# Kernel optimization log

Hardware: AMD Instinct MI355X
Metric: run time of the kernel (lower is better)

Reference implementation:

```python
import jax, jax.numpy as jnp
import numpy as np

ORDER = 256
THETA = 1024.0
HIDDEN = 512
FEAT = 128
BATCH = 64
SEQ = 1025  # loop consumes steps 1..SEQ-1 -> T = 1024 outputs
LEAKY_SLOPE = 0.2  # tf.nn.leaky_relu default alpha


def _expm_np(M):
    # scaling-and-squaring + Taylor, float64, sufficient for the LMU A matrix
    n = max(0, int(np.ceil(np.log2(max(1.0, np.linalg.norm(M, 1))))) + 4)
    A = M / (2.0 ** n)
    E = np.eye(M.shape[0])
    term = np.eye(M.shape[0])
    for k in range(1, 24):
        term = term @ A / k
        E = E + term
    for _ in range(n):
        E = E @ E
    return E


def get_state_space_matrices(order, theta):
    Q = np.arange(order, dtype=np.float64)
    R = (2 * Q + 1)[:, None] / theta
    j, i = np.meshgrid(Q, Q)
    Ac = np.where(i < j, -1, (-1.0) ** (i - j + 1)) * R
    Bc = (-1.0) ** Q[:, None] * R
    # zero-order-hold discretization with dt=1 (matches scipy cont2discrete zoh)
    Ad = _expm_np(Ac)
    Bd = np.linalg.solve(Ac, (Ad - np.eye(order)) @ Bc)
    return Ad.astype(np.float32), Bd.astype(np.float32)


def _glorot(key, shape):
    fan_in, fan_out = shape[0], shape[1]
    lim = np.sqrt(6.0 / (fan_in + fan_out))
    return jax.random.uniform(key, shape, jnp.float32, -lim, lim)


def setup_inputs() -> dict:
    key = jax.random.key(0)
    ks = jax.random.split(key, 6)
    A_np, B_np = get_state_space_matrices(ORDER, THETA)
    return {
        "x": jax.random.normal(ks[0], (BATCH, SEQ, FEAT), jnp.float32),
        "A": jnp.asarray(A_np),            # (order, order)
        "Bv": jnp.asarray(B_np),           # (order, 1)
        "W_x": _glorot(ks[1], (FEAT, HIDDEN)),
        "e_x": _glorot(ks[2], (FEAT, 1)),
        "W_h": _glorot(ks[3], (HIDDEN, HIDDEN)),
        "W_m": _glorot(ks[4], (HIDDEN, ORDER)),
    }


def reference(x, A, Bv, W_x, e_x, W_h, W_m):
    B, S, F = x.shape
    order = A.shape[0]
    hidden_dim = W_h.shape[0]
    b_row = Bv[:, 0]  # (order,)

    def step(carry, x_t):
        m, h = carry                       # m: (B, order), h: (B, hidden)
        u = x_t @ e_x                      # (B, 1)
        m = m @ A.T + b_row[None, :] * u   # A@m + B*u  -> (B, order)
        h = x_t @ W_x + h @ W_h.T + m @ W_m.T
        h = jnp.where(h >= 0, h, LEAKY_SLOPE * h)  # leaky_relu(alpha=0.2)
        return (m, h), h

    m0 = jnp.zeros((B, order), jnp.float32)
    h0 = jnp.zeros((B, hidden_dim), jnp.float32)
    xs = jnp.swapaxes(x[:, 1:, :], 0, 1)   # (T, B, F); step 0 is skipped as in the source
    _, hs = jax.lax.scan(step, (m0, h0), xs)
    return jnp.swapaxes(hs, 0, 1)          # (B, T, hidden)
```

## Files before the change

### kernel.cpp

```cpp
#include <hip/hip_runtime.h>
#include <stdint.h>


typedef _Float16 half8 __attribute__((ext_vector_type(8)));
typedef float f32x4 __attribute__((ext_vector_type(4)));
typedef unsigned int u32x4 __attribute__((ext_vector_type(4)));
typedef unsigned int u32x2 __attribute__((ext_vector_type(2)));

union H8 { half8 h; unsigned int u[4]; };
union F16 { u32x4 q; half8 h; };

#define MFMA16(a, b, c) __builtin_amdgcn_mfma_f32_16x16x32_f16((a), (b), (c), 0, 0, 0)
#define ASTORE64(p, v) __hip_atomic_store((unsigned long long*)(p), (v), \
                                          __ATOMIC_RELAXED, __HIP_MEMORY_SCOPE_AGENT)

__device__ __forceinline__ half8 ld_frag16(const _Float16* W, size_t foff) {
    F16 r;
    r.q = *(const u32x4*)(W + foff);
    return r.h;
}

__device__ __forceinline__ void unpack8(u32x4 A, u32x4 B, half8& hi, half8& lo) {
    H8 h, l;
    h.u[0] = (A[0] & 0xffffu) | (A[1] << 16);  l.u[0] = (A[0] >> 16) | (A[1] & 0xffff0000u);
    h.u[1] = (A[2] & 0xffffu) | (A[3] << 16);  l.u[1] = (A[2] >> 16) | (A[3] & 0xffff0000u);
    h.u[2] = (B[0] & 0xffffu) | (B[1] << 16);  l.u[2] = (B[0] >> 16) | (B[1] & 0xffff0000u);
    h.u[3] = (B[2] & 0xffffu) | (B[3] << 16);  l.u[3] = (B[2] >> 16) | (B[3] & 0xffff0000u);
    hi = h.h; lo = l.h;
}

__global__ void k_prep(const float* __restrict__ A, const float* __restrict__ W_x,
                       const float* __restrict__ W_h, const float* __restrict__ W_m,
                       _Float16* __restrict__ Whi, _Float16* __restrict__ Wlo,
                       _Float16* __restrict__ WxThi, _Float16* __restrict__ WxTlo,
                       float* __restrict__ WmT, float* __restrict__ AT) {
    int bid = blockIdx.x, tid = threadIdx.x;
    if (bid < 512) {
        int r = bid;
        for (int c = tid; c < 512; c += 256) {
            float v = W_h[(size_t)r * 512 + c];
            _Float16 hi = (_Float16)v;
            _Float16 lo = (_Float16)(v - (float)hi);
            int cb = c >> 5, w = c & 31;
            int kgi = (w & 15) >> 2;
            int e = (w & 3) + ((w & 16) ? 4 : 0);
            size_t idx = (((size_t)r * 16 + cb) * 4 + kgi) * 8 + e;
            Whi[idx] = hi;
            Wlo[idx] = lo;
        }
    } else if (bid < 1024) {
        int n = bid - 512;
        if (tid < 128) {
            int f = tid;
            float v = W_x[(size_t)f * 512 + n];
            _Float16 hi = (_Float16)v;
            _Float16 lo = (_Float16)(v - (float)hi);
            int kt = f >> 5, w = f & 31;
            int kgi = (w & 15) >> 2;
            int e = (w & 3) + ((w & 16) ? 4 : 0);
            size_t idx = (((size_t)n * 4 + kt) * 4 + kgi) * 8 + e;
            WxThi[idx] = hi;
            WxTlo[idx] = lo;
        }
    } else if (bid < 1280) {
        int d = bid - 1024;
        for (int n = tid; n < 512; n += 256)
            WmT[(size_t)d * 512 + n] = W_m[(size_t)n * 256 + d];
    } else {
        int e = bid - 1280;
        if (tid < 256) AT[(size_t)e * 256 + tid] = A[(size_t)tid * 256 + e];
    }
}

__global__ void k_u(const float* __restrict__ x, const float* __restrict__ e_x,
                    float* __restrict__ u) {
    int wave = threadIdx.x >> 6, l = threadIdx.x & 63;
    int t = blockIdx.x * 4 + wave;
    int b = blockIdx.y;
    const float* xr = x + ((size_t)b * 1025 + t + 1) * 128;
    float s = xr[2 * l] * e_x[2 * l] + xr[2 * l + 1] * e_x[2 * l + 1];
#pragma unroll
    for (int off = 1; off < 64; off <<= 1) s += __shfl_xor(s, off);
    if (l == 0) u[(size_t)b * 1024 + t] = s;
}

__global__ void k_a64(const float* __restrict__ S, float* __restrict__ D,
                      float* __restrict__ DT, int writeT) {
    int r = blockIdx.x, c = threadIdx.x;
    float acc = 0.f;
    for (int e = 0; e < 256; ++e)
        acc += S[(size_t)r * 256 + e] * S[(size_t)e * 256 + c];
    D[(size_t)r * 256 + c] = acc;
    if (writeT) DT[(size_t)c * 256 + r] = acc;
}

__global__ void k_vk(const float* __restrict__ AT, const float* __restrict__ Bv,
                     float* __restrict__ V) {
    __shared__ float cur[256];
    int tid = threadIdx.x;
    cur[tid] = Bv[tid];
    V[tid] = cur[tid];
    __syncthreads();
    for (int k = 1; k < 64; ++k) {
        float nv = 0.f;
        for (int e = 0; e < 256; ++e) nv += AT[(size_t)e * 256 + tid] * cur[e];
        __syncthreads();
        cur[tid] = nv;
        V[(size_t)k * 256 + tid] = nv;
        __syncthreads();
    }
}

__global__ void k_vchain(const float* __restrict__ A64T, float* __restrict__ V) {
    __shared__ float cur[256];
    int j = blockIdx.x, d = threadIdx.x;
    cur[d] = V[(size_t)j * 256 + d];
    __syncthreads();
    for (int c = 1; c < 16; ++c) {
        float nv = 0.f;
        for (int e = 0; e < 256; ++e) nv += A64T[(size_t)e * 256 + d] * cur[e];
        __syncthreads();
        cur[d] = nv;
        V[((size_t)c * 64 + j) * 256 + d] = nv;
        __syncthreads();
    }
}

__global__ void k_c(const float* __restrict__ V, const float* __restrict__ WmT,
                    _Float16* __restrict__ CThi) {
    int k = blockIdx.x, n = threadIdx.x;
    const float* vk = V + (size_t)k * 256;
    float acc = 0.f;
    for (int d = 0; d < 256; ++d) acc += vk[d] * WmT[(size_t)d * 512 + n];
    int ck = k >> 5, w = k & 31;
    int kgi = (w & 15) >> 2;
    int e = (w & 3) + ((w & 16) ? 4 : 0);
    CThi[(((size_t)n * 32 + ck) * 4 + kgi) * 8 + e] = (_Float16)acc;
}

__global__ __launch_bounds__(256, 1) void k_preconv(const float* __restrict__ x,
                                                    const float* __restrict__ u,
                                                    const _Float16* __restrict__ WxThi,
                                                    const _Float16* __restrict__ WxTlo,
                                                    const _Float16* __restrict__ CThi,
                                                    float* __restrict__ out) {
    __shared__ float xt[64][132];
    __shared__ float ut[1088];
    int tid = threadIdx.x;
    int Mb = blockIdx.x, Nb = blockIdx.y;
    int b = Mb >> 4;
    int t0 = (Mb & 15) * 64;
    const float* src = x + ((size_t)b * 1025 + t0 + 1) * 128;
#pragma unroll
    for (int i = 0; i < 8; ++i) {
        int idx = tid + i * 256;
        int row = idx >> 5, c4 = (idx & 31) * 4;
        *(f32x4*)&xt[row][c4] = *(const f32x4*)(src + (size_t)row * 128 + c4);
    }
    for (int i = tid; i < 1088; i += 256) {
        int tau = t0 - 1024 + i;
        ut[i] = (tau >= 0) ? u[(size_t)b * 1024 + tau] : 0.f;
    }
    __syncthreads();

    int wave = tid >> 6, l = tid & 63;
    int kg4 = l >> 4, kg = kg4 * 4;
    int mrow = wave * 16 + (l & 15);

    half8 ah[4], al[4];
#pragma unroll
    for (int kt = 0; kt < 4; ++kt) {
        f32x4 f0 = *(const f32x4*)&xt[mrow][kt * 32 + kg];
        f32x4 f1 = *(const f32x4*)&xt[mrow][kt * 32 + kg + 16];
        H8 hh, ll;
#pragma unroll
        for (int e = 0; e < 4; ++e) {
            _Float16 h0 = (_Float16)f0[e];
            ((_Float16*)&hh)[e] = h0;
            ((_Float16*)&ll)[e] = (_Float16)(f0[e] - (float)h0);
            _Float16 h1 = (_Float16)f1[e];
            ((_Float16*)&hh)[e + 4] = h1;
            ((_Float16*)&ll)[e + 4] = (_Float16)(f1[e] - (float)h1);
        }
        ah[kt] = hh.h;
        al[kt] = ll.h;
    }

    f32x4 acc[16];
#pragma unroll
    for (int nt = 0; nt < 16; ++nt) acc[nt] = (f32x4)0.f;

#pragma unroll
    for (int nt = 0; nt < 16; ++nt) {
        size_t nrow = (size_t)(Nb * 256 + nt * 16 + (l & 15));
#pragma unroll
        for (int kt = 0; kt < 4; ++kt) {
            size_t fo = (((nrow * 4 + kt) * 4 + kg4)) * 8;
            half8 bh = ld_frag16(WxThi, fo);
            half8 bl = ld_frag16(WxTlo, fo);
            acc[nt] = MFMA16(ah[kt], bh, acc[nt]);
            acc[nt] = MFMA16(al[kt], bh, acc[nt]);
            acc[nt] = MFMA16(ah[kt], bl, acc[nt]);
        }
    }

    for (int ck = 0; ck < 32; ++ck) {
        int base0 = mrow + 1024 - ck * 32 - kg;
        H8 au;
#pragma unroll
        for (int e = 0; e < 4; ++e) {
            ((_Float16*)&au)[e] = (_Float16)ut[base0 - e];
            ((_Float16*)&au)[e + 4] = (_Float16)ut[base0 - 16 - e];
        }
#pragma unroll
        for (int nt = 0; nt < 16; ++nt) {
            size_t nrow = (size_t)(Nb * 256 + nt * 16 + (l & 15));
            half8 bh = ld_frag16(CThi, (((nrow * 32 + ck) * 4 + kg4)) * 8);
            acc[nt] = MFMA16(au.h, bh, acc[nt]);
        }
    }

#pragma unroll
    for (int nt = 0; nt < 16; ++nt) {
#pragma unroll
        for (int r = 0; r < 4; ++r) {
            size_t bt = (size_t)Mb * 64 + wave * 16 + 4 * (l >> 4) + r;
            out[bt * 512 + Nb * 256 + nt * 16 + (l & 15)] = acc[nt][r];
        }
    }
}

#define TSTATE_U32 (64 * 512 * 2)

#define LD8W(p, v0, v1, v2, v3, v4, v5, v6, v7)                                   \
    asm volatile("global_load_dwordx4 %0, %8, off\n\t"                            \
                 "global_load_dwordx4 %1, %8, off offset:64\n\t"                  \
                 "global_load_dwordx4 %2, %8, off offset:128\n\t"                 \
                 "global_load_dwordx4 %3, %8, off offset:192\n\t"                 \
                 "global_load_dwordx4 %4, %8, off offset:256\n\t"                 \
                 "global_load_dwordx4 %5, %8, off offset:320\n\t"                 \
                 "global_load_dwordx4 %6, %8, off offset:384\n\t"                 \
                 "global_load_dwordx4 %7, %8, off offset:448"                     \
                 : "=&v"(v0), "=&v"(v1), "=&v"(v2), "=&v"(v3), "=&v"(v4),         \
                   "=&v"(v5), "=&v"(v6), "=&v"(v7)                                \
                 : "v"(p))

#define BC8(x) __builtin_bit_cast(half8, x)

__global__ __launch_bounds__(512, 1) void k_seq(const _Float16* __restrict__ Whi,
                                                const _Float16* __restrict__ Wlo,
                                                unsigned int* sbuf, float* out) {
    __shared__ unsigned int sval[16 * 512];
    __shared__ f32x4 pex[8][64];
    int tid = threadIdx.x;
    int w = tid >> 6, l = tid & 63;
    int g = blockIdx.x >> 2, rank = blockIdx.x & 3;
    int kh = w >> 2;
    int kbase = kh * 256;
    int kg4 = l >> 4, kg = kg4 * 4;
    int rowBase = rank * 128;

    u32x4 h0_0, h0_1, h0_2, h0_3, h0_4, h0_5, h0_6, h0_7;
    u32x4 h1_0, h1_1, h1_2, h1_3, h1_4, h1_5, h1_6, h1_7;
    u32x4 l0_0, l0_1, l0_2, l0_3, l0_4, l0_5, l0_6, l0_7;
    u32x4 l1_0, l1_1, l1_2, l1_3, l1_4, l1_5, l1_6, l1_7;
    {
        int rowA = rowBase + (w & 3) * 32 + (l & 15);
        int rowB = rowA + 16;
        int cb0 = kh * 8;
        size_t foA = (((size_t)rowA * 16 + cb0) * 4 + kg4) * 8;
        size_t foB = (((size_t)rowB * 16 + cb0) * 4 + kg4) * 8;
        LD8W(Whi + foA, h0_0, h0_1, h0_2, h0_3, h0_4, h0_5, h0_6, h0_7);
        LD8W(Whi + foB, h1_0, h1_1, h1_2, h1_3, h1_4, h1_5, h1_6, h1_7);
        LD8W(Wlo + foA, l0_0, l0_1, l0_2, l0_3, l0_4, l0_5, l0_6, l0_7);
        LD8W(Wlo + foB, l1_0, l1_1, l1_2, l1_3, l1_4, l1_5, l1_6, l1_7);
        asm volatile("s_waitcnt vmcnt(0)" ::: "memory");
    }

    int frow = rowBase + (w & 3) * 32 + kh * 16 + (l & 15);
    int bX = ((l & 15) & 7) << 2;
    int bloc = 2 * w + (l >> 5);
    unsigned int sX = (unsigned int)((bloc & 7) << 2);
    int lam = l & 31;

#pragma unroll 1
    for (int t = 1; t <= 1024; ++t) {
        float pxw[4];
#pragma unroll
        for (int r = 0; r < 4; ++r) {
            int bG = g * 16 + 4 * (l >> 4) + r;
            pxw[r] = out[(((size_t)bG << 10) + (t - 1)) * 512 + frow];
        }

        const unsigned int* rb = sbuf + (size_t)((t - 1) & 1) * TSTATE_U32;
        const unsigned int* pL =
            rb + (size_t)(g * 16 + bloc) * 1024 + (size_t)lam * 4;
        u32x4 e0, e1, e2, e3, e4, e5, e6, e7;
        unsigned int exp = (unsigned int)(t - 1);
        int rounds = 0;
        for (;;) {
            asm volatile(
                "global_load_dwordx4 %0, %8, off sc1\n\t"
                "global_load_dwordx4 %1, %8, off offset:512 sc1\n\t"
                "global_load_dwordx4 %2, %8, off offset:1024 sc1\n\t"
                "global_load_dwordx4 %3, %8, off offset:1536 sc1\n\t"
                "global_load_dwordx4 %4, %8, off offset:2048 sc1\n\t"
                "global_load_dwordx4 %5, %8, off offset:2560 sc1\n\t"
                "global_load_dwordx4 %6, %8, off offset:3072 sc1\n\t"
                "global_load_dwordx4 %7, %8, off offset:3584 sc1\n\t"
                "s_waitcnt vmcnt(0)"
                : "=&v"(e0), "=&v"(e1), "=&v"(e2), "=&v"(e3),
                  "=&v"(e4), "=&v"(e5), "=&v"(e6), "=&v"(e7)
                : "v"(pL) : "memory");
            unsigned int bad =
                (e0[1] ^ exp) | (e0[3] ^ exp) | (e1[1] ^ exp) | (e1[3] ^ exp) |
                (e2[1] ^ exp) | (e2[3] ^ exp) | (e3[1] ^ exp) | (e3[3] ^ exp) |
                (e4[1] ^ exp) | (e4[3] ^ exp) | (e5[1] ^ exp) | (e5[3] ^ exp) |
                (e6[1] ^ exp) | (e6[3] ^ exp) | (e7[1] ^ exp) | (e7[3] ^ exp);
            if (__all(bad == 0)) break;
            if (++rounds > 200000) break;
        }

        {
            unsigned int* row = sval + bloc * 512;
            int kb = 2 * lam;
            *(u32x2*)&row[(kb)       ^ sX] = (u32x2){e0[0], e0[2]};
            *(u32x2*)&row[(kb + 64)  ^ sX] = (u32x2){e1[0], e1[2]};
            *(u32x2*)&row[(kb + 128) ^ sX] = (u32x2){e2[0], e2[2]};
            *(u32x2*)&row[(kb + 192) ^ sX] = (u32x2){e3[0], e3[2]};
            *(u32x2*)&row[(kb + 256) ^ sX] = (u32x2){e4[0], e4[2]};
            *(u32x2*)&row[(kb + 320) ^ sX] = (u32x2){e5[0], e5[2]};
            *(u32x2*)&row[(kb + 384) ^ sX] = (u32x2){e6[0], e6[2]};
            *(u32x2*)&row[(kb + 448) ^ sX] = (u32x2){e7[0], e7[2]};
        }
        __syncthreads();

        const unsigned int* brow = sval + (l & 15) * 512;
        f32x4 acc0 = (f32x4)0.f, acc1 = (f32x4)0.f;
#define RSTEP(KT, BH0, BL0, BH1, BL1)                                             \
        {                                                                         \
            int k0 = kbase + (KT) * 32 + kg;                                      \
            u32x4 qa = *(const u32x4*)&brow[k0 ^ bX];                             \
            u32x4 qb = *(const u32x4*)&brow[(k0 + 16) ^ bX];                      \
            half8 Ah, Al;                                                         \
            unpack8(qa, qb, Ah, Al);                                              \
            acc0 = MFMA16(Ah, BC8(BH0), acc0);                                    \
            acc0 = MFMA16(Al, BC8(BH0), acc0);                                    \
            acc0 = MFMA16(Ah, BC8(BL0), acc0);                                    \
            acc1 = MFMA16(Ah, BC8(BH1), acc1);                                    \
            acc1 = MFMA16(Al, BC8(BH1), acc1);                                    \
            acc1 = MFMA16(Ah, BC8(BL1), acc1);                                    \
        }
        RSTEP(0, h0_0, l0_0, h1_0, l1_0);
        RSTEP(1, h0_1, l0_1, h1_1, l1_1);
        RSTEP(2, h0_2, l0_2, h1_2, l1_2);
        RSTEP(3, h0_3, l0_3, h1_3, l1_3);
        RSTEP(4, h0_4, l0_4, h1_4, l1_4);
        RSTEP(5, h0_5, l0_5, h1_5, l1_5);
        RSTEP(6, h0_6, l0_6, h1_6, l1_6);
        RSTEP(7, h0_7, l0_7, h1_7, l1_7);
#undef RSTEP

        pex[w][l] = kh ? acc0 : acc1;
        __syncthreads();
        f32x4 sum = (kh ? acc1 : acc0) + pex[w ^ 4][l];

        unsigned int* wbuf = sbuf + (size_t)(t & 1) * TSTATE_U32;
        float vout[4];
#pragma unroll
        for (int r = 0; r < 4; ++r) {
            int bG = g * 16 + 4 * (l >> 4) + r;
            float v = sum[r] + pxw[r];
            v = (v >= 0.f) ? v : 0.2f * v;
            vout[r] = v;
            _Float16 hi = (_Float16)v;
            _Float16 lo = (_Float16)(v - (float)hi);
            unsigned int pr = (unsigned int)__builtin_bit_cast(unsigned short, hi) |
                              ((unsigned int)__builtin_bit_cast(unsigned short, lo) << 16);
            unsigned long long ev =
                (unsigned long long)pr | ((unsigned long long)(unsigned int)t << 32);
            ASTORE64(wbuf + ((size_t)bG * 512 + frow) * 2, ev);
        }
#pragma unroll
        for (int r = 0; r < 4; ++r) {
            int bG = g * 16 + 4 * (l >> 4) + r;
            out[(((size_t)bG << 10) + (t - 1)) * 512 + frow] = vout[r];
        }
    }
}

extern "C" void kernel_launch(void* const* d_in, const int* in_sizes, int n_in,
                              void* d_out, int out_size, void* d_ws, size_t ws_size,
                              hipStream_t stream) {
    const float* x   = (const float*)d_in[0];
    const float* A   = (const float*)d_in[1];
    const float* Bv  = (const float*)d_in[2];
    const float* W_x = (const float*)d_in[3];
    const float* e_x = (const float*)d_in[4];
    const float* W_h = (const float*)d_in[5];
    const float* W_m = (const float*)d_in[6];
    float* out = (float*)d_out;

    char* ws = (char*)d_ws;
    size_t off = 0;
    auto carve = [&](size_t n) -> char* {
        char* p = ws + off;
        off += (n + 255) & ~(size_t)255;
        return p;
    };
    _Float16* Whi   = (_Float16*)carve(512 * 512 * 2);
    _Float16* Wlo   = (_Float16*)carve(512 * 512 * 2);
    _Float16* WxThi = (_Float16*)carve(512 * 128 * 2);
    _Float16* WxTlo = (_Float16*)carve(512 * 128 * 2);
    float* WmT      = (float*)carve(256 * 512 * 4);
    float* AT       = (float*)carve(256 * 256 * 4);
    float* u        = (float*)carve(64 * 1024 * 4);
    unsigned int* sbuf = (unsigned int*)carve((size_t)2 * TSTATE_U32 * 4);
    float* Apw0     = (float*)carve(256 * 256 * 4);
    float* Apw1     = (float*)carve(256 * 256 * 4);
    float* A64T     = (float*)carve(256 * 256 * 4);
    float* V        = (float*)carve(1024 * 256 * 4);
    _Float16* CThi  = (_Float16*)carve(512 * 1024 * 2);

    hipMemsetAsync(sbuf, 0, (size_t)2 * TSTATE_U32 * 4, stream);

    hipLaunchKernelGGL(k_prep, dim3(1536), dim3(256), 0, stream, A, W_x, W_h, W_m,
                       Whi, Wlo, WxThi, WxTlo, WmT, AT);
    hipLaunchKernelGGL(k_u, dim3(256, 64), dim3(256), 0, stream, x, e_x, u);

    hipLaunchKernelGGL(k_a64, dim3(256), dim3(256), 0, stream, A, Apw0, A64T, 0);
    hipLaunchKernelGGL(k_a64, dim3(256), dim3(256), 0, stream, Apw0, Apw1, A64T, 0);
    hipLaunchKernelGGL(k_a64, dim3(256), dim3(256), 0, stream, Apw1, Apw0, A64T, 0);
    hipLaunchKernelGGL(k_a64, dim3(256), dim3(256), 0, stream, Apw0, Apw1, A64T, 0);
    hipLaunchKernelGGL(k_a64, dim3(256), dim3(256), 0, stream, Apw1, Apw0, A64T, 0);
    hipLaunchKernelGGL(k_a64, dim3(256), dim3(256), 0, stream, Apw0, Apw1, A64T, 1);

    hipLaunchKernelGGL(k_vk, dim3(1), dim3(256), 0, stream, AT, Bv, V);
    hipLaunchKernelGGL(k_vchain, dim3(64), dim3(256), 0, stream, A64T, V);
    hipLaunchKernelGGL(k_c, dim3(1024), dim3(512), 0, stream, V, WmT, CThi);

    hipLaunchKernelGGL(k_preconv, dim3(1024, 2), dim3(256), 0, stream, x, u,
                       WxThi, WxTlo, CThi, out);

    void* args[] = {(void*)&Whi, (void*)&Wlo, (void*)&sbuf, (void*)&out};
    hipLaunchCooperativeKernel((void*)k_seq, dim3(16), dim3(512), args, 0, stream);
}
```

Measured before the change: 5.483 ms.

## Split recurrent step across 32 blocks and prefetch next state speculatively

Launches the cooperative sequential kernel on 32 blocks instead of 16, so each block owns 64 hidden rows and each wave computes one 16-row MFMA tile with half the weight registers. The split-K halves now finalize two batch rows each, instead of the reduction result being used redundantly. The next step's state poll is issued right after the tagged stores, so the first load overlaps with the output store and loop overhead and is usually already complete. In exchange there are more blocks exchanging state through global memory each step, and a speculative first load that may come back stale and need a retry.

```diff
diff --git a/kernel.cpp b/kernel.cpp
--- a/kernel.cpp
+++ b/kernel.cpp
@@ -245,6 +245,31 @@
                    "=&v"(v5), "=&v"(v6), "=&v"(v7)                                \
                  : "v"(p))
 
+#define ISSUE_STATE(p)                                                            \
+    asm volatile("global_load_dwordx4 %0, %8, off sc1\n\t"                        \
+                 "global_load_dwordx4 %1, %8, off offset:512 sc1\n\t"             \
+                 "global_load_dwordx4 %2, %8, off offset:1024 sc1\n\t"            \
+                 "global_load_dwordx4 %3, %8, off offset:1536 sc1\n\t"            \
+                 "global_load_dwordx4 %4, %8, off offset:2048 sc1\n\t"            \
+                 "global_load_dwordx4 %5, %8, off offset:2560 sc1\n\t"            \
+                 "global_load_dwordx4 %6, %8, off offset:3072 sc1\n\t"            \
+                 "global_load_dwordx4 %7, %8, off offset:3584 sc1"                \
+                 : "=&v"(e0), "=&v"(e1), "=&v"(e2), "=&v"(e3),                    \
+                   "=&v"(e4), "=&v"(e5), "=&v"(e6), "=&v"(e7)                     \
+                 : "v"(p) : "memory")
+
+#define VM0_FENCE()                                                               \
+    do {                                                                          \
+        asm volatile("s_waitcnt vmcnt(0)" ::: "memory");                          \
+        __builtin_amdgcn_sched_barrier(0);                                        \
+    } while (0)
+
+#define TAGBAD(exp)                                                               \
+    ((e0[1] ^ (exp)) | (e0[3] ^ (exp)) | (e1[1] ^ (exp)) | (e1[3] ^ (exp)) |      \
+     (e2[1] ^ (exp)) | (e2[3] ^ (exp)) | (e3[1] ^ (exp)) | (e3[3] ^ (exp)) |      \
+     (e4[1] ^ (exp)) | (e4[3] ^ (exp)) | (e5[1] ^ (exp)) | (e5[3] ^ (exp)) |      \
+     (e6[1] ^ (exp)) | (e6[3] ^ (exp)) | (e7[1] ^ (exp)) | (e7[3] ^ (exp)))
+
 #define BC8(x) __builtin_bit_cast(half8, x)
 
 __global__ __launch_bounds__(512, 1) void k_seq(const _Float16* __restrict__ Whi,
@@ -254,71 +279,50 @@
     __shared__ f32x4 pex[8][64];
     int tid = threadIdx.x;
     int w = tid >> 6, l = tid & 63;
-    int g = blockIdx.x >> 2, rank = blockIdx.x & 3;
+    int g = blockIdx.x >> 3, rank = blockIdx.x & 7;
     int kh = w >> 2;
     int kbase = kh * 256;
     int kg4 = l >> 4, kg = kg4 * 4;
-    int rowBase = rank * 128;
-
-    u32x4 h0_0, h0_1, h0_2, h0_3, h0_4, h0_5, h0_6, h0_7;
-    u32x4 h1_0, h1_1, h1_2, h1_3, h1_4, h1_5, h1_6, h1_7;
-    u32x4 l0_0, l0_1, l0_2, l0_3, l0_4, l0_5, l0_6, l0_7;
-    u32x4 l1_0, l1_1, l1_2, l1_3, l1_4, l1_5, l1_6, l1_7;
+
+    u32x4 wh0, wh1, wh2, wh3, wh4, wh5, wh6, wh7;
+    u32x4 wl0, wl1, wl2, wl3, wl4, wl5, wl6, wl7;
+    int frow = rank * 64 + (w & 3) * 16 + (l & 15);
     {
-        int rowA = rowBase + (w & 3) * 32 + (l & 15);
-        int rowB = rowA + 16;
-        int cb0 = kh * 8;
-        size_t foA = (((size_t)rowA * 16 + cb0) * 4 + kg4) * 8;
-        size_t foB = (((size_t)rowB * 16 + cb0) * 4 + kg4) * 8;
-        LD8W(Whi + foA, h0_0, h0_1, h0_2, h0_3, h0_4, h0_5, h0_6, h0_7);
-        LD8W(Whi + foB, h1_0, h1_1, h1_2, h1_3, h1_4, h1_5, h1_6, h1_7);
-        LD8W(Wlo + foA, l0_0, l0_1, l0_2, l0_3, l0_4, l0_5, l0_6, l0_7);
-        LD8W(Wlo + foB, l1_0, l1_1, l1_2, l1_3, l1_4, l1_5, l1_6, l1_7);
+        size_t fo = (((size_t)frow * 16 + kh * 8) * 4 + kg4) * 8;
+        LD8W(Whi + fo, wh0, wh1, wh2, wh3, wh4, wh5, wh6, wh7);
+        LD8W(Wlo + fo, wl0, wl1, wl2, wl3, wl4, wl5, wl6, wl7);
         asm volatile("s_waitcnt vmcnt(0)" ::: "memory");
     }
 
-    int frow = rowBase + (w & 3) * 32 + kh * 16 + (l & 15);
     int bX = ((l & 15) & 7) << 2;
     int bloc = 2 * w + (l >> 5);
     unsigned int sX = (unsigned int)((bloc & 7) << 2);
     int lam = l & 31;
+    size_t soff = (size_t)(g * 16 + bloc) * 1024 + (size_t)lam * 4;
+
+    u32x4 e0, e1, e2, e3, e4, e5, e6, e7;
+    ISSUE_STATE(sbuf + soff);
 
 #pragma unroll 1
     for (int t = 1; t <= 1024; ++t) {
-        float pxw[4];
-#pragma unroll
-        for (int r = 0; r < 4; ++r) {
-            int bG = g * 16 + 4 * (l >> 4) + r;
-            pxw[r] = out[(((size_t)bG << 10) + (t - 1)) * 512 + frow];
-        }
-
-        const unsigned int* rb = sbuf + (size_t)((t - 1) & 1) * TSTATE_U32;
-        const unsigned int* pL =
-            rb + (size_t)(g * 16 + bloc) * 1024 + (size_t)lam * 4;
-        u32x4 e0, e1, e2, e3, e4, e5, e6, e7;
+        float pxw0, pxw1;
+        {
+            int r0 = 2 * kh;
+            int bG0 = g * 16 + 4 * (l >> 4) + r0;
+            pxw0 = out[(((size_t)bG0 << 10) + (t - 1)) * 512 + frow];
+            pxw1 = out[(((size_t)(bG0 + 1) << 10) + (t - 1)) * 512 + frow];
+        }
+
+        const unsigned int* pL = sbuf + (size_t)((t - 1) & 1) * TSTATE_U32 + soff;
         unsigned int exp = (unsigned int)(t - 1);
+        VM0_FENCE();
+        unsigned int bad = TAGBAD(exp);
         int rounds = 0;
-        for (;;) {
-            asm volatile(
-                "global_load_dwordx4 %0, %8, off sc1\n\t"
-                "global_load_dwordx4 %1, %8, off offset:512 sc1\n\t"
-                "global_load_dwordx4 %2, %8, off offset:1024 sc1\n\t"
-                "global_load_dwordx4 %3, %8, off offset:1536 sc1\n\t"
-                "global_load_dwordx4 %4, %8, off offset:2048 sc1\n\t"
-                "global_load_dwordx4 %5, %8, off offset:2560 sc1\n\t"
-                "global_load_dwordx4 %6, %8, off offset:3072 sc1\n\t"
-                "global_load_dwordx4 %7, %8, off offset:3584 sc1\n\t"
-                "s_waitcnt vmcnt(0)"
-                : "=&v"(e0), "=&v"(e1), "=&v"(e2), "=&v"(e3),
-                  "=&v"(e4), "=&v"(e5), "=&v"(e6), "=&v"(e7)
-                : "v"(pL) : "memory");
-            unsigned int bad =
-                (e0[1] ^ exp) | (e0[3] ^ exp) | (e1[1] ^ exp) | (e1[3] ^ exp) |
-                (e2[1] ^ exp) | (e2[3] ^ exp) | (e3[1] ^ exp) | (e3[3] ^ exp) |
-                (e4[1] ^ exp) | (e4[3] ^ exp) | (e5[1] ^ exp) | (e5[3] ^ exp) |
-                (e6[1] ^ exp) | (e6[3] ^ exp) | (e7[1] ^ exp) | (e7[3] ^ exp);
-            if (__all(bad == 0)) break;
+        while (!__all(bad == 0)) {
             if (++rounds > 200000) break;
+            ISSUE_STATE(pL);
+            VM0_FENCE();
+            bad = TAGBAD(exp);
         }
 
         {
@@ -336,56 +340,55 @@
         __syncthreads();
 
         const unsigned int* brow = sval + (l & 15) * 512;
-        f32x4 acc0 = (f32x4)0.f, acc1 = (f32x4)0.f;
-#define RSTEP(KT, BH0, BL0, BH1, BL1)                                             \
+        f32x4 acc = (f32x4)0.f;
+#define RSTEP(KT, BH, BL)                                                         \
         {                                                                         \
             int k0 = kbase + (KT) * 32 + kg;                                      \
             u32x4 qa = *(const u32x4*)&brow[k0 ^ bX];                             \
             u32x4 qb = *(const u32x4*)&brow[(k0 + 16) ^ bX];                      \
             half8 Ah, Al;                                                         \
             unpack8(qa, qb, Ah, Al);                                              \
-            acc0 = MFMA16(Ah, BC8(BH0), acc0);                                    \
-            acc0 = MFMA16(Al, BC8(BH0), acc0);                                    \
-            acc0 = MFMA16(Ah, BC8(BL0), acc0);                                    \
-            acc1 = MFMA16(Ah, BC8(BH1), acc1);                                    \
-            acc1 = MFMA16(Al, BC8(BH1), acc1);                                    \
-            acc1 = MFMA16(Ah, BC8(BL1), acc1);                                    \
-        }
-        RSTEP(0, h0_0, l0_0, h1_0, l1_0);
-        RSTEP(1, h0_1, l0_1, h1_1, l1_1);
-        RSTEP(2, h0_2, l0_2, h1_2, l1_2);
-        RSTEP(3, h0_3, l0_3, h1_3, l1_3);
-        RSTEP(4, h0_4, l0_4, h1_4, l1_4);
-        RSTEP(5, h0_5, l0_5, h1_5, l1_5);
-        RSTEP(6, h0_6, l0_6, h1_6, l1_6);
-        RSTEP(7, h0_7, l0_7, h1_7, l1_7);
+            acc = MFMA16(Ah, BC8(BH), acc);                                       \
+            acc = MFMA16(Al, BC8(BH), acc);                                       \
+            acc = MFMA16(Ah, BC8(BL), acc);                                       \
+        }
+        RSTEP(0, wh0, wl0);
+        RSTEP(1, wh1, wl1);
+        RSTEP(2, wh2, wl2);
+        RSTEP(3, wh3, wl3);
+        RSTEP(4, wh4, wl4);
+        RSTEP(5, wh5, wl5);
+        RSTEP(6, wh6, wl6);
+        RSTEP(7, wh7, wl7);
 #undef RSTEP
 
-        pex[w][l] = kh ? acc0 : acc1;
-        __syncthreads();
-        f32x4 sum = (kh ? acc1 : acc0) + pex[w ^ 4][l];
-
+        pex[w][l] = acc;
+        __syncthreads();
+        f32x4 sum = acc + pex[w ^ 4][l];
+
+        float s0 = kh ? sum[2] : sum[0];
+        float s1 = kh ? sum[3] : sum[1];
         unsigned int* wbuf = sbuf + (size_t)(t & 1) * TSTATE_U32;
-        float vout[4];
-#pragma unroll
-        for (int r = 0; r < 4; ++r) {
-            int bG = g * 16 + 4 * (l >> 4) + r;
-            float v = sum[r] + pxw[r];
-            v = (v >= 0.f) ? v : 0.2f * v;
-            vout[r] = v;
-            _Float16 hi = (_Float16)v;
-            _Float16 lo = (_Float16)(v - (float)hi);
-            unsigned int pr = (unsigned int)__builtin_bit_cast(unsigned short, hi) |
-                              ((unsigned int)__builtin_bit_cast(unsigned short, lo) << 16);
-            unsigned long long ev =
-                (unsigned long long)pr | ((unsigned long long)(unsigned int)t << 32);
-            ASTORE64(wbuf + ((size_t)bG * 512 + frow) * 2, ev);
-        }
-#pragma unroll
-        for (int r = 0; r < 4; ++r) {
-            int bG = g * 16 + 4 * (l >> 4) + r;
-            out[(((size_t)bG << 10) + (t - 1)) * 512 + frow] = vout[r];
-        }
+        int bG0 = g * 16 + 4 * (l >> 4) + 2 * kh;
+        float v0 = s0 + pxw0;
+        v0 = (v0 >= 0.f) ? v0 : 0.2f * v0;
+        float v1 = s1 + pxw1;
+        v1 = (v1 >= 0.f) ? v1 : 0.2f * v1;
+        {
+            _Float16 hi0 = (_Float16)v0, lo0 = (_Float16)(v0 - (float)hi0);
+            _Float16 hi1 = (_Float16)v1, lo1 = (_Float16)(v1 - (float)hi1);
+            unsigned int p0 = (unsigned int)__builtin_bit_cast(unsigned short, hi0) |
+                              ((unsigned int)__builtin_bit_cast(unsigned short, lo0) << 16);
+            unsigned int p1 = (unsigned int)__builtin_bit_cast(unsigned short, hi1) |
+                              ((unsigned int)__builtin_bit_cast(unsigned short, lo1) << 16);
+            unsigned long long t64 = (unsigned long long)(unsigned int)t << 32;
+            ASTORE64(wbuf + ((size_t)bG0 * 512 + frow) * 2, (unsigned long long)p0 | t64);
+            ASTORE64(wbuf + ((size_t)(bG0 + 1) * 512 + frow) * 2,
+                     (unsigned long long)p1 | t64);
+        }
+        ISSUE_STATE(sbuf + (size_t)(t & 1) * TSTATE_U32 + soff);
+        out[(((size_t)bG0 << 10) + (t - 1)) * 512 + frow] = v0;
+        out[(((size_t)(bG0 + 1) << 10) + (t - 1)) * 512 + frow] = v1;
     }
 }
 
@@ -443,5 +446,5 @@
                        WxThi, WxTlo, CThi, out);
 
     void* args[] = {(void*)&Whi, (void*)&Wlo, (void*)&sbuf, (void*)&out};
-    hipLaunchCooperativeKernel((void*)k_seq, dim3(16), dim3(512), args, 0, stream);
-}
+    hipLaunchCooperativeKernel((void*)k_seq, dim3(32), dim3(512), args, 0, stream);
+}
```

Result: faster. 5.217 ms (-4.9%).
